# Performance work log

Hardware: AMD Instinct MI355X
Metric: run time of the kernel (lower is better)

Reference implementation:

```python
import jax, jax.numpy as jnp
import numpy as np

VOCAB = 50257
HIDDEN = 16
B, T = 256, 8192


def setup_inputs() -> dict:
    key = jax.random.key(0)
    ks = jax.random.split(key, 8)
    seq = jax.random.randint(ks[0], (B, T), 0, VOCAB, dtype=jnp.int64 if jax.config.jax_enable_x64 else jnp.int32)
    s = 1.0 / np.sqrt(HIDDEN)
    return {
        "seq": seq,
        "embed": jax.random.normal(ks[1], (VOCAB, HIDDEN), jnp.float32) * 0.02,
        # nn.Linear(hidden, 1): weight [1,hidden] -> stored transposed [hidden,1]
        "Wg": jax.random.uniform(ks[2], (HIDDEN, 1), jnp.float32, -s, s),
        "bg": jax.random.uniform(ks[3], (1,), jnp.float32, -s, s),
        # nn.Linear(hidden, hidden) -> [hidden, hidden] (transposed)
        "Wu": jax.random.uniform(ks[4], (HIDDEN, HIDDEN), jnp.float32, -s, s),
        "bu": jax.random.uniform(ks[5], (HIDDEN,), jnp.float32, -s, s),
        # nn.Linear(hidden, vocab) -> [hidden, vocab] (transposed)
        "Wo": jax.random.uniform(ks[6], (HIDDEN, VOCAB), jnp.float32, -s, s),
        "bo": jax.random.uniform(ks[7], (VOCAB,), jnp.float32, -s, s),
    }


def reference(seq, embed, Wg, bg, Wu, bu, Wo, bo):
    # The torch loop is a purely additive recurrence:
    #   memory = sum_t sigmoid(gate(x_t)) * tanh(update(x_t))
    # so we batch all timesteps and do one masked-free sum over T.
    x = embed[seq]                                  # [B, T, H] gather
    g = jax.nn.sigmoid(jnp.einsum("bth,ho->bto", x, Wg) + bg)   # [B, T, 1]
    new_content = jnp.tanh(jnp.einsum("bth,hk->btk", x, Wu) + bu)  # [B, T, H]
    memory = jnp.sum(g * new_content, axis=1)       # [B, H]
    return memory @ Wo + bo                         # [B, vocab]
```

## Files before the change

### kernel.cpp

```cpp
#include <hip/hip_runtime.h>
#include <cmath>

#define VOCAB   50257
#define HIDDEN  16
#define BATCH   256
#define SEQLEN  8192
#define TCHUNKS 8
#define K3_BCHUNK 16
#define K3_VPT   4

__device__ __forceinline__ float ub0(unsigned x){ return (float)( x        & 0xffu); }
__device__ __forceinline__ float ub1(unsigned x){ return (float)((x >> 8 ) & 0xffu); }
__device__ __forceinline__ float ub2(unsigned x){ return (float)((x >> 16) & 0xffu); }
__device__ __forceinline__ float ub3(unsigned x){ return (float)( x >> 24        ); }

__global__ __launch_bounds__(256) void k1_build_table(
    const float* __restrict__ embed, const float* __restrict__ Wg,
    const float* __restrict__ bg,    const float* __restrict__ Wu,
    const float* __restrict__ bu,    unsigned* __restrict__ ctab,
    float* __restrict__ mem_acc)
{
    __shared__ float sWu[256], sWg[16], sbu[16];
    const int tid = threadIdx.x;
    sWu[tid] = Wu[tid];
    if (tid < 16) { sWg[tid] = Wg[tid]; sbu[tid] = bu[tid]; }
    if (blockIdx.x < (BATCH * HIDDEN) / 256)
        mem_acc[blockIdx.x * 256 + tid] = 0.f;
    __syncthreads();

    const int v = blockIdx.x * 256 + tid;
    if (v >= VOCAB) return;

    const float4* er = (const float4*)(embed + (size_t)v * HIDDEN);
    float4 e0 = er[0], e1 = er[1], e2 = er[2], e3 = er[3];
    float e[16] = {e0.x,e0.y,e0.z,e0.w, e1.x,e1.y,e1.z,e1.w,
                   e2.x,e2.y,e2.z,e2.w, e3.x,e3.y,e3.z,e3.w};

    float z = bg[0];
#pragma unroll
    for (int h = 0; h < 16; ++h) z = fmaf(e[h], sWg[h], z);
    const float g = 1.0f / (1.0f + __expf(-z));

    float o[16];
#pragma unroll
    for (int k = 0; k < 16; ++k) {
        float u = sbu[k];
#pragma unroll
        for (int h = 0; h < 16; ++h) u = fmaf(e[h], sWu[h * 16 + k], u);
        o[k] = g * (1.f - 2.f / (__expf(2.f * u) + 1.f));
    }

    unsigned d[4];
#pragma unroll
    for (int j = 0; j < 4; ++j) {
        unsigned q0 = (unsigned)fmaf(o[4*j+0], 127.f, 128.5f);
        unsigned q1 = (unsigned)fmaf(o[4*j+1], 127.f, 128.5f);
        unsigned q2 = (unsigned)fmaf(o[4*j+2], 127.f, 128.5f);
        unsigned q3 = (unsigned)fmaf(o[4*j+3], 127.f, 128.5f);
        d[j] = q0 | (q1 << 8) | (q2 << 16) | (q3 << 24);
    }
    ((uint4*)(ctab + (size_t)v * 4))[0] = make_uint4(d[0], d[1], d[2], d[3]);
}

__global__ __launch_bounds__(256) void k2_accum(
    const int* __restrict__ seq, const unsigned* __restrict__ ctab,
    float* __restrict__ mem_acc)
{
    const int b = blockIdx.x, chunk = blockIdx.y, tid = threadIdx.x;
    constexpr int TPC = SEQLEN / TCHUNKS;
    const int* srow = seq + (size_t)b * SEQLEN + (size_t)chunk * TPC;
    const int sub = tid & 1;
    const int tok = tid >> 1;

    float r[8];
#pragma unroll
    for (int j = 0; j < 8; ++j) r[j] = 0.f;

#pragma unroll
    for (int i = 0; i < TPC / 128; ++i) {
        const int idx = __builtin_nontemporal_load(srow + i * 128 + tok);
        const uint2 p = ((const uint2*)(ctab + (size_t)idx * 4))[sub];
        r[0] += ub0(p.x); r[1] += ub1(p.x); r[2] += ub2(p.x); r[3] += ub3(p.x);
        r[4] += ub0(p.y); r[5] += ub1(p.y); r[6] += ub2(p.y); r[7] += ub3(p.y);
    }

    constexpr float S = 1.f / 127.f;
#pragma unroll
    for (int j = 0; j < 8; ++j)
        r[j] = fmaf(r[j], S, -(float)(TPC / 128) * 128.f * S);

#pragma unroll
    for (int off = 2; off < 64; off <<= 1)
#pragma unroll
        for (int j = 0; j < 8; ++j) r[j] += __shfl_xor(r[j], off, 64);

    __shared__ float red[4][16];
    const int lane = tid & 63, wave = tid >> 6;
    if (lane < 2) {
#pragma unroll
        for (int j = 0; j < 8; ++j) red[wave][lane * 8 + j] = r[j];
    }
    __syncthreads();
    if (tid < 16) {
        atomicAdd(&mem_acc[(size_t)b * HIDDEN + tid],
                  red[0][tid] + red[1][tid] + red[2][tid] + red[3][tid]);
    }
}

__global__ __launch_bounds__(256) void k3_output(
    const float* __restrict__ mem_acc, const float* __restrict__ Wo,
    const float* __restrict__ bo,      float* __restrict__ out)
{
    __shared__ float smem[K3_BCHUNK * 16];
    const int tid = threadIdx.x;
    const int b0 = blockIdx.y * K3_BCHUNK;
    smem[tid] = mem_acc[(size_t)b0 * HIDDEN + tid];
    __syncthreads();

    const int vbase = blockIdx.x * (256 * K3_VPT) + tid;
    bool valid[K3_VPT];
    int  vc[K3_VPT];
#pragma unroll
    for (int c = 0; c < K3_VPT; ++c) {
        const int v = vbase + c * 256;
        valid[c] = v < VOCAB;
        vc[c] = valid[c] ? v : 0;
    }

    float w[16][K3_VPT];
#pragma unroll
    for (int h = 0; h < 16; ++h)
#pragma unroll
        for (int c = 0; c < K3_VPT; ++c)
            w[h][c] = Wo[(size_t)h * VOCAB + vc[c]];
    float bias[K3_VPT];
#pragma unroll
    for (int c = 0; c < K3_VPT; ++c) bias[c] = bo[vc[c]];

#pragma unroll
    for (int bl = 0; bl < K3_BCHUNK; ++bl) {
        float acc[K3_VPT] = {bias[0], bias[1], bias[2], bias[3]};
#pragma unroll
        for (int h = 0; h < 16; ++h) {
            const float mv = smem[bl * 16 + h];
#pragma unroll
            for (int c = 0; c < K3_VPT; ++c)
                acc[c] = fmaf(mv, w[h][c], acc[c]);
        }
        float* orow = out + (size_t)(b0 + bl) * VOCAB;
#pragma unroll
        for (int c = 0; c < K3_VPT; ++c)
            if (valid[c]) __builtin_nontemporal_store(acc[c], &orow[vc[c]]);
    }
}

extern "C" void kernel_launch(void* const* d_in, const int* in_sizes, int n_in,
                              void* d_out, int out_size, void* d_ws, size_t ws_size,
                              hipStream_t stream) {
    const int*   seq   = (const int*)  d_in[0];
    const float* embed = (const float*)d_in[1];
    const float* Wg    = (const float*)d_in[2];
    const float* bg    = (const float*)d_in[3];
    const float* Wu    = (const float*)d_in[4];
    const float* bu    = (const float*)d_in[5];
    const float* Wo    = (const float*)d_in[6];
    const float* bo    = (const float*)d_in[7];
    float* out = (float*)d_out;

    unsigned* ctab   = (unsigned*)d_ws;
    float*    mem_acc = (float*)(ctab + (size_t)VOCAB * 4);

    k1_build_table<<<dim3((VOCAB + 255) / 256), 256, 0, stream>>>(
        embed, Wg, bg, Wu, bu, ctab, mem_acc);
    k2_accum<<<dim3(BATCH, TCHUNKS), 256, 0, stream>>>(seq, ctab, mem_acc);
    k3_output<<<dim3((VOCAB + 256 * K3_VPT - 1) / (256 * K3_VPT),
                     BATCH / K3_BCHUNK), 256, 0, stream>>>(
        mem_acc, Wo, bo, out);
}
```

Before: 116.8 us.

## Fuse table build, accumulation and output into one cooperative persistent kernel

Replaces the three separate launches with a single cooperative kernel of 1024 blocks that runs the table-build, token-accumulation and output-projection phases separated by grid-wide syncs. Each block also prefetches its Wo slice into registers before the first grid sync, so that load overlaps the accumulation phase. The aim is to remove launch gaps and tail effects between kernels. In exchange it adds grid.sync costs and register pressure from holding 64 weights across phases, and it falls back to the old three-kernel path if the cooperative launch fails.

```diff
diff --git a/kernel.cpp b/kernel.cpp
--- a/kernel.cpp
+++ b/kernel.cpp
@@ -1,5 +1,8 @@
 #include <hip/hip_runtime.h>
+#include <hip/hip_cooperative_groups.h>
 #include <cmath>
+
+namespace cg = cooperative_groups;
 
 #define VOCAB   50257
 #define HIDDEN  16
@@ -9,26 +12,32 @@
 #define K3_BCHUNK 16
 #define K3_VPT   4
 
+#define FUSED_BLOCKS 1024
+#define K1_BLOCKS    ((VOCAB + 255) / 256)
+#define K3_VBLOCKS   ((VOCAB + 256 * K3_VPT - 1) / (256 * K3_VPT))
+#define K3_UNITS     (K3_VBLOCKS * (BATCH / K3_BCHUNK))
+
 __device__ __forceinline__ float ub0(unsigned x){ return (float)( x        & 0xffu); }
 __device__ __forceinline__ float ub1(unsigned x){ return (float)((x >> 8 ) & 0xffu); }
 __device__ __forceinline__ float ub2(unsigned x){ return (float)((x >> 16) & 0xffu); }
 __device__ __forceinline__ float ub3(unsigned x){ return (float)( x >> 24        ); }
 
-__global__ __launch_bounds__(256) void k1_build_table(
+
+__device__ __forceinline__ void k1_phase(
+    int bx, int tid,
     const float* __restrict__ embed, const float* __restrict__ Wg,
     const float* __restrict__ bg,    const float* __restrict__ Wu,
     const float* __restrict__ bu,    unsigned* __restrict__ ctab,
-    float* __restrict__ mem_acc)
-{
-    __shared__ float sWu[256], sWg[16], sbu[16];
-    const int tid = threadIdx.x;
+    float* __restrict__ mem_acc, float* sWu, float* sWg, float* sbu)
+{
+    if (bx < (BATCH * HIDDEN) / 256)
+        mem_acc[bx * 256 + tid] = 0.f;
+    if (bx >= K1_BLOCKS) return;
     sWu[tid] = Wu[tid];
     if (tid < 16) { sWg[tid] = Wg[tid]; sbu[tid] = bu[tid]; }
-    if (blockIdx.x < (BATCH * HIDDEN) / 256)
-        mem_acc[blockIdx.x * 256 + tid] = 0.f;
     __syncthreads();
 
-    const int v = blockIdx.x * 256 + tid;
+    const int v = bx * 256 + tid;
     if (v >= VOCAB) return;
 
     const float4* er = (const float4*)(embed + (size_t)v * HIDDEN);
@@ -62,11 +71,11 @@
     ((uint4*)(ctab + (size_t)v * 4))[0] = make_uint4(d[0], d[1], d[2], d[3]);
 }
 
-__global__ __launch_bounds__(256) void k2_accum(
+__device__ __forceinline__ void k2_phase(
+    int b, int chunk, int tid,
     const int* __restrict__ seq, const unsigned* __restrict__ ctab,
-    float* __restrict__ mem_acc)
-{
-    const int b = blockIdx.x, chunk = blockIdx.y, tid = threadIdx.x;
+    float* __restrict__ mem_acc, float (*red)[16])
+{
     constexpr int TPC = SEQLEN / TCHUNKS;
     const int* srow = seq + (size_t)b * SEQLEN + (size_t)chunk * TPC;
     const int sub = tid & 1;
@@ -94,7 +103,6 @@
 #pragma unroll
         for (int j = 0; j < 8; ++j) r[j] += __shfl_xor(r[j], off, 64);
 
-    __shared__ float red[4][16];
     const int lane = tid & 63, wave = tid >> 6;
     if (lane < 2) {
 #pragma unroll
@@ -105,6 +113,96 @@
         atomicAdd(&mem_acc[(size_t)b * HIDDEN + tid],
                   red[0][tid] + red[1][tid] + red[2][tid] + red[3][tid]);
     }
+}
+
+__global__ __launch_bounds__(256, 4) void fused_all(
+    const int* __restrict__ seq, const float* __restrict__ embed,
+    const float* __restrict__ Wg, const float* __restrict__ bg,
+    const float* __restrict__ Wu, const float* __restrict__ bu,
+    const float* __restrict__ Wo, const float* __restrict__ bo,
+    unsigned* __restrict__ ctab,  float* __restrict__ mem_acc,
+    float* __restrict__ out)
+{
+    __shared__ float sA[256 + 16 + 16];
+    __shared__ float red[4][16];
+    __shared__ float smem[K3_BCHUNK * 16];
+
+    const int tid = threadIdx.x, bx = blockIdx.x;
+    cg::grid_group grid = cg::this_grid();
+
+    k1_phase(bx, tid, embed, Wg, bg, Wu, bu, ctab, mem_acc,
+             sA, sA + 256, sA + 272);
+
+    const bool cact = bx < K3_UNITS;
+    const int vb = cact ? bx % K3_VBLOCKS : 0;
+    const int b0 = (cact ? bx / K3_VBLOCKS : 0) * K3_BCHUNK;
+    const int vbase = vb * (256 * K3_VPT) + tid;
+    bool valid[K3_VPT];
+    int  vc[K3_VPT];
+    float w[16][K3_VPT], bias[K3_VPT];
+    if (cact) {
+#pragma unroll
+        for (int c = 0; c < K3_VPT; ++c) {
+            const int v = vbase + c * 256;
+            valid[c] = v < VOCAB;
+            vc[c] = valid[c] ? v : 0;
+        }
+#pragma unroll
+        for (int h = 0; h < 16; ++h)
+#pragma unroll
+            for (int c = 0; c < K3_VPT; ++c)
+                w[h][c] = Wo[(size_t)h * VOCAB + vc[c]];
+#pragma unroll
+        for (int c = 0; c < K3_VPT; ++c) bias[c] = bo[vc[c]];
+    }
+
+    grid.sync();
+
+    for (int u = bx; u < BATCH * TCHUNKS; u += FUSED_BLOCKS) {
+        k2_phase(u >> 3, u & 7, tid, seq, ctab, mem_acc, red);
+        __syncthreads();
+    }
+
+    grid.sync();
+
+    if (cact) {
+        smem[tid] = mem_acc[(size_t)b0 * HIDDEN + tid];
+        __syncthreads();
+#pragma unroll
+        for (int bl = 0; bl < K3_BCHUNK; ++bl) {
+            float acc[K3_VPT] = {bias[0], bias[1], bias[2], bias[3]};
+#pragma unroll
+            for (int h = 0; h < 16; ++h) {
+                const float mv = smem[bl * 16 + h];
+#pragma unroll
+                for (int c = 0; c < K3_VPT; ++c)
+                    acc[c] = fmaf(mv, w[h][c], acc[c]);
+            }
+            float* orow = out + (size_t)(b0 + bl) * VOCAB;
+#pragma unroll
+            for (int c = 0; c < K3_VPT; ++c)
+                if (valid[c]) __builtin_nontemporal_store(acc[c], &orow[vc[c]]);
+        }
+    }
+}
+
+__global__ __launch_bounds__(256) void k1_build_table(
+    const float* __restrict__ embed, const float* __restrict__ Wg,
+    const float* __restrict__ bg,    const float* __restrict__ Wu,
+    const float* __restrict__ bu,    unsigned* __restrict__ ctab,
+    float* __restrict__ mem_acc)
+{
+    __shared__ float sA[256 + 16 + 16];
+    k1_phase(blockIdx.x, threadIdx.x, embed, Wg, bg, Wu, bu, ctab, mem_acc,
+             sA, sA + 256, sA + 272);
+}
+
+__global__ __launch_bounds__(256) void k2_accum(
+    const int* __restrict__ seq, const unsigned* __restrict__ ctab,
+    float* __restrict__ mem_acc)
+{
+    __shared__ float red[4][16];
+    k2_phase(blockIdx.x, blockIdx.y, threadIdx.x, seq, ctab, mem_acc, red);
 }
 
 __global__ __launch_bounds__(256) void k3_output(
@@ -167,13 +265,22 @@
     const float* bo    = (const float*)d_in[7];
     float* out = (float*)d_out;
 
-    unsigned* ctab   = (unsigned*)d_ws;
+    unsigned* ctab    = (unsigned*)d_ws;
     float*    mem_acc = (float*)(ctab + (size_t)VOCAB * 4);
 
-    k1_build_table<<<dim3((VOCAB + 255) / 256), 256, 0, stream>>>(
-        embed, Wg, bg, Wu, bu, ctab, mem_acc);
-    k2_accum<<<dim3(BATCH, TCHUNKS), 256, 0, stream>>>(seq, ctab, mem_acc);
-    k3_output<<<dim3((VOCAB + 256 * K3_VPT - 1) / (256 * K3_VPT),
-                     BATCH / K3_BCHUNK), 256, 0, stream>>>(
-        mem_acc, Wo, bo, out);
-}
+    void* kargs[] = {
+        (void*)&seq, (void*)&embed, (void*)&Wg, (void*)&bg, (void*)&Wu,
+        (void*)&bu, (void*)&Wo, (void*)&bo, (void*)&ctab, (void*)&mem_acc,
+        (void*)&out
+    };
+    hipError_t err = hipLaunchCooperativeKernel(
+        (const void*)fused_all, dim3(FUSED_BLOCKS), dim3(256), kargs, 0, stream);
+    if (err != hipSuccess) {
+        (void)hipGetLastError();
+        k1_build_table<<<dim3(K1_BLOCKS), 256, 0, stream>>>(
+            embed, Wg, bg, Wu, bu, ctab, mem_acc);
+        k2_accum<<<dim3(BATCH, TCHUNKS), 256, 0, stream>>>(seq, ctab, mem_acc);
+        k3_output<<<dim3(K3_VBLOCKS, BATCH / K3_BCHUNK), 256, 0, stream>>>(
+            mem_acc, Wo, bo, out);
+    }
+}
```

Result: slower. 379.3 us (+224.8%).
